# Kernel tuning notes

Hardware: AMD Instinct MI355X
Metric: run time of the kernel (lower is better)

## Reference

```python
import jax, jax.numpy as jnp
import numpy as np

GAMMA = 1.0

def setup_inputs() -> dict:
    key = jax.random.key(0)
    kx, ky = jax.random.split(key)
    x = jax.random.normal(kx, (8192, 512), dtype=jnp.float32)
    y = jax.random.normal(ky, (8192, 512), dtype=jnp.float32)
    return {"x": x, "y": y}

def reference(x, y):
    # RBF kernel K[i,j] = exp(-gamma * ||x_i - y_j||^2)
    # O(N*M*D) broadcasted diff tensor (128GB at these sizes).
    x_sq = jnp.sum(x * x, axis=-1)                      # [N]
    y_sq = jnp.sum(y * y, axis=-1)                      # [M]
    xy = jnp.einsum('nd,md->nm', x, y)                  # [N,M] GEMM
    sq_norm = x_sq[:, None] + y_sq[None, :] - 2.0 * xy
    sq_norm = jnp.maximum(sq_norm, 0.0)                 # guard fp cancellation
    return jnp.exp(-GAMMA * sq_norm)
```

## Files before the change

kernel.cpp:

```cpp
#include <hip/hip_runtime.h>


typedef int i32x8 __attribute__((ext_vector_type(8)));
typedef float f32x16 __attribute__((ext_vector_type(16)));

#define NROWS 8192
#define DIM 512
#define NKT 4

__device__ __forceinline__ unsigned char f2e4m3(float f) {
  unsigned u = __float_as_uint(f);
  unsigned sign = (u >> 24) & 0x80u;
  int e = (int)((u >> 23) & 0xFF);
  unsigned m = u & 0x7FFFFFu;
  if (e >= 127 + 9) return sign | 0x7E;
  if (e < 127 - 6) {
    if (e < 127 - 10) return (unsigned char)sign;
    unsigned full = 0x800000u | m;
    int div = 20 + (127 - 6 - e);
    unsigned q = full >> div;
    unsigned rem = full & ((1u << div) - 1u);
    unsigned half = 1u << (div - 1);
    q += (rem > half) || (rem == half && (q & 1));
    return (unsigned char)(sign | q);
  }
  unsigned q = m >> 20;
  unsigned rem = m & 0xFFFFFu;
  q += (rem > 0x80000u) || (rem == 0x80000u && (q & 1));
  unsigned ef = (unsigned)(e - 120);
  if (q == 8) { q = 0; ef++; }
  if (ef > 15 || (ef == 15 && q == 7)) return sign | 0x7E;
  return (unsigned char)(sign | (ef << 3) | q);
}

__device__ __forceinline__ void gload_lds16(const void* g, void* l) {
  __builtin_amdgcn_global_load_lds(
      (const __attribute__((address_space(1))) void*)g,
      (__attribute__((address_space(3))) void*)l, 16, 0, 0);
}

__device__ __forceinline__ f32x16 mfma_mx(i32x8 a, i32x8 b, f32x16 c) {
  return __builtin_amdgcn_mfma_scale_f32_32x32x64_f8f6f4(
      a, b, c, 0, 0, 0, 0x7F7F7F7Fu, 0, 0x7F7F7F7Fu);
}

__device__ __forceinline__ i32x8 lds_frag8(const unsigned char* hb, int R, int s0) {
  const int r7 = R & 7;
  int4 lo = *(const int4*)(hb + R * 128 + ((s0 ^ r7) << 4));
  int4 hi = *(const int4*)(hb + R * 128 + (((s0 + 1) ^ r7) << 4));
  i32x8 v;
  v[0] = lo.x; v[1] = lo.y; v[2] = lo.z; v[3] = lo.w;
  v[4] = hi.x; v[5] = hi.y; v[6] = hi.z; v[7] = hi.w;
  return v;
}

__global__ void rbf_prep(const float* __restrict__ x, const float* __restrict__ y,
                         unsigned char* __restrict__ xb, unsigned char* __restrict__ yb,
                         float* __restrict__ xsq, float* __restrict__ ysq) {
  int wave = threadIdx.x >> 6;
  int lane = threadIdx.x & 63;
  int row = blockIdx.x * 4 + wave;
  const float* src;
  unsigned char* dst;
  float* sq;
  int r;
  if (row < NROWS) { src = x; dst = xb; sq = xsq; r = row; }
  else             { src = y; dst = yb; sq = ysq; r = row - NROWS; }

  const float4* p = (const float4*)(src + (size_t)r * DIM);
  float4 v0 = p[lane * 2];
  float4 v1 = p[lane * 2 + 1];
  float s = v0.x * v0.x + v0.y * v0.y + v0.z * v0.z + v0.w * v0.w
          + v1.x * v1.x + v1.y * v1.y + v1.z * v1.z + v1.w * v1.w;

  union { uint2 u; unsigned char b[8]; } o;
  o.b[0] = f2e4m3(v0.x); o.b[1] = f2e4m3(v0.y);
  o.b[2] = f2e4m3(v0.z); o.b[3] = f2e4m3(v0.w);
  o.b[4] = f2e4m3(v1.x); o.b[5] = f2e4m3(v1.y);
  o.b[6] = f2e4m3(v1.z); o.b[7] = f2e4m3(v1.w);
  *(uint2*)(dst + (size_t)r * DIM + lane * 8) = o.u;

  #pragma unroll
  for (int off = 32; off > 0; off >>= 1) s += __shfl_down(s, off);
  if (lane == 0) sq[r] = s;
}

__global__ __launch_bounds__(512, 2) void rbf_gemm(
    const unsigned char* __restrict__ xb, const unsigned char* __restrict__ yb,
    const float* __restrict__ xsq, const float* __restrict__ ysq,
    float* __restrict__ out) {
  __shared__ __align__(16) unsigned char lds[2][2][2][128 * 128];

  const int t = threadIdx.x;
  const int lane = t & 63;
  const int w = t >> 6;
  const int wr = w >> 2;
  const int wc = w & 3;
  const int l31 = lane & 31;
  const int hi2 = lane >> 5;

  const int bx = blockIdx.x & 31;
  const int by = blockIdx.x >> 5;
  const size_t arow0 = (size_t)by * 256;
  const size_t brow0 = (size_t)bx * 256;

#define STAGE_HALF(d, ab, h, kt)                                            \
  {                                                                         \
    const unsigned char* gsrc_ = (ab) ? yb : xb;                            \
    const size_t grow0_ = ((ab) ? brow0 : arow0) + (h) * 128;               \
    _Pragma("unroll")                                                       \
    for (int r_ = 0; r_ < 2; ++r_) {                                        \
      const int c_ = r_ * 512 + t;                       \
      const int row_ = c_ >> 3;                                 \
      const int ss_ = c_ & 7;                                               \
      gload_lds16(gsrc_ + (grow0_ + row_) * DIM + (kt) * 128 +              \
                      ((ss_ ^ (row_ & 7)) << 4),                            \
                  &lds[d][ab][h][c_ * 16]);                                 \
    }                                                                       \
  }

#define MFMA_Q(afr, bfr, nt)                                                \
  _Pragma("unroll")                                                         \
  for (int m_ = 0; m_ < 4; ++m_)                                            \
    acc[m_][nt] = mfma_mx(afr[m_], bfr[nt], acc[m_][nt]);

  f32x16 acc[4][2] = {};

  STAGE_HALF(0, 0, 0, 0);
  STAGE_HALF(0, 0, 1, 0);
  STAGE_HALF(0, 1, 0, 0);
  STAGE_HALF(0, 1, 1, 0);
  STAGE_HALF(1, 0, 0, 1);
  STAGE_HALF(1, 0, 1, 1);
  asm volatile("s_waitcnt vmcnt(4)" ::: "memory");
  __builtin_amdgcn_sched_barrier(0);
  __builtin_amdgcn_s_barrier();

  #pragma unroll
  for (int kt = 0; kt < NKT; ++kt) {
    const int d = kt & 1;
    const unsigned char* Ah = lds[d][0][wr];
    const unsigned char* Bh = lds[d][1][wc >> 1];
    const int Rb = (wc & 1) * 64;

    const bool stB = kt + 1 < NKT;
    const bool stA = kt + 2 < NKT;
    const int dB = (kt + 1) & 1;

    i32x8 a0[4], a1[4], b0[2], b1[2];

    #pragma unroll
    for (int m = 0; m < 4; ++m) a0[m] = lds_frag8(Ah, m * 32 + l31, hi2 * 2);
    #pragma unroll
    for (int n = 0; n < 2; ++n)
      b0[n] = lds_frag8(Bh, Rb + n * 32 + l31, hi2 * 2);
    if (stB) STAGE_HALF(dB, 1, 0, kt + 1);
    __builtin_amdgcn_s_barrier();
    asm volatile("s_waitcnt lgkmcnt(0)" ::: "memory");
    __builtin_amdgcn_sched_barrier(0);
    __builtin_amdgcn_s_setprio(1);
    MFMA_Q(a0, b0, 0);
    __builtin_amdgcn_s_setprio(0);
    __builtin_amdgcn_s_barrier();

    #pragma unroll
    for (int m = 0; m < 4; ++m)
      a1[m] = lds_frag8(Ah, m * 32 + l31, 4 + hi2 * 2);
    #pragma unroll
    for (int n = 0; n < 2; ++n)
      b1[n] = lds_frag8(Bh, Rb + n * 32 + l31, 4 + hi2 * 2);
    if (stB) STAGE_HALF(dB, 1, 1, kt + 1);
    __builtin_amdgcn_s_barrier();
    asm volatile("s_waitcnt lgkmcnt(0)" ::: "memory");
    __builtin_amdgcn_sched_barrier(0);
    __builtin_amdgcn_s_setprio(1);
    MFMA_Q(a0, b0, 1);
    __builtin_amdgcn_s_setprio(0);
    __builtin_amdgcn_s_barrier();

    if (stA) STAGE_HALF(d, 0, 0, kt + 2);
    __builtin_amdgcn_s_barrier();
    __builtin_amdgcn_s_setprio(1);
    MFMA_Q(a1, b1, 0);
    __builtin_amdgcn_s_setprio(0);
    __builtin_amdgcn_s_barrier();

    if (stA) STAGE_HALF(d, 0, 1, kt + 2);
    __builtin_amdgcn_s_barrier();
    __builtin_amdgcn_s_setprio(1);
    MFMA_Q(a1, b1, 1);
    __builtin_amdgcn_s_setprio(0);
    if (stA) {
      asm volatile("s_waitcnt vmcnt(4)" ::: "memory");
    } else if (stB) {
      asm volatile("s_waitcnt vmcnt(0)" ::: "memory");
    }
    __builtin_amdgcn_sched_barrier(0);
    if (kt + 1 < NKT) __builtin_amdgcn_s_barrier();
  }

  const size_t orow0 = arow0 + wr * 128;
  const size_t ocol0 = brow0 + wc * 64;

  float ysv[2];
  #pragma unroll
  for (int n = 0; n < 2; ++n) ysv[n] = ysq[ocol0 + n * 32 + l31];

  #pragma unroll
  for (int mt = 0; mt < 4; ++mt) {
    #pragma unroll
    for (int j = 0; j < 16; ++j) {
      const int rl = (j & 3) + 8 * (j >> 2) + 4 * hi2;
      const size_t row = orow0 + mt * 32 + rl;
      const float xsv = xsq[row];
      #pragma unroll
      for (int n = 0; n < 2; ++n) {
        float v = xsv + ysv[n] - 2.0f * acc[mt][n][j];
        v = fmaxf(v, 0.0f);
        out[row * (size_t)NROWS + ocol0 + n * 32 + l31] = __expf(-v);
      }
    }
  }
}

__global__ void rbf_naive(const float* __restrict__ x, const float* __restrict__ y,
                          float* __restrict__ out) {
  int j = blockIdx.x * 16 + (threadIdx.x & 15);
  int i = blockIdx.y * 16 + (threadIdx.x >> 4);
  const float4* xp = (const float4*)(x + (size_t)i * DIM);
  const float4* yp = (const float4*)(y + (size_t)j * DIM);
  float s = 0.f;
  for (int k = 0; k < DIM / 4; ++k) {
    float4 a = xp[k], b = yp[k];
    float d0 = a.x - b.x, d1 = a.y - b.y, d2 = a.z - b.z, d3 = a.w - b.w;
    s += d0 * d0 + d1 * d1 + d2 * d2 + d3 * d3;
  }
  out[(size_t)i * NROWS + j] = __expf(-fmaxf(s, 0.0f));
}

extern "C" void kernel_launch(void* const* d_in, const int* in_sizes, int n_in,
                              void* d_out, int out_size, void* d_ws, size_t ws_size,
                              hipStream_t stream) {
  const float* x = (const float*)d_in[0];
  const float* y = (const float*)d_in[1];
  float* out = (float*)d_out;

  const size_t need = (size_t)8 * 1024 * 1024 + 64 * 1024;
  if (ws_size >= need) {
    unsigned char* xb = (unsigned char*)d_ws;
    unsigned char* yb = xb + (size_t)NROWS * DIM;
    float* xsq = (float*)((char*)d_ws + (size_t)8 * 1024 * 1024);
    float* ysq = xsq + NROWS;

    rbf_prep<<<(2 * NROWS) / 4, 256, 0, stream>>>(x, y, xb, yb, xsq, ysq);
    rbf_gemm<<<(NROWS / 256) * (NROWS / 256), 512, 0, stream>>>(xb, yb, xsq, ysq, out);
  } else {
    dim3 grid(NROWS / 16, NROWS / 16);
    rbf_naive<<<grid, 256, 0, stream>>>(x, y, out);
  }
}
```

Baseline: 88.49 us.

## Shrink GEMM tile to 128x128 with simple double-buffered pipeline and XCD-aware block remap

Changes the output tile from 256x256 with 512 threads to 128x128 with 256 threads, giving 4096 blocks instead of 1024. The hand-tuned ping-pong schedule with setprio and partial vmcnt waits is replaced by a plain double buffer with __syncthreads. Block IDs are remapped across the 8 XCDs so neighbouring tiles land on the same XCD for L2 reuse. The kernel is dominated by writing the 256MB fp32 output, so more, smaller blocks may balance the store traffic better. The cost is more redundant operand loads and less overlap between loads and MFMAs.

After: 93.30 us. +5.4%, slower.

```diff
diff --git a/kernel.cpp b/kernel.cpp
--- a/kernel.cpp
+++ b/kernel.cpp
@@ -44,10 +44,10 @@
       a, b, c, 0, 0, 0, 0x7F7F7F7Fu, 0, 0x7F7F7F7Fu);
 }
 
-__device__ __forceinline__ i32x8 lds_frag8(const unsigned char* hb, int R, int s0) {
+__device__ __forceinline__ i32x8 lds_frag8(const unsigned char* tb, int R, int s0) {
   const int r7 = R & 7;
-  int4 lo = *(const int4*)(hb + R * 128 + ((s0 ^ r7) << 4));
-  int4 hi = *(const int4*)(hb + R * 128 + (((s0 + 1) ^ r7) << 4));
+  int4 lo = *(const int4*)(tb + R * 128 + ((s0 ^ r7) << 4));
+  int4 hi = *(const int4*)(tb + R * 128 + (((s0 + 1) ^ r7) << 4));
   i32x8 v;
   v[0] = lo.x; v[1] = lo.y; v[2] = lo.z; v[3] = lo.w;
   v[4] = hi.x; v[5] = hi.y; v[6] = hi.z; v[7] = hi.w;
@@ -85,139 +85,99 @@
   if (lane == 0) sq[r] = s;
 }
 
-__global__ __launch_bounds__(512, 2) void rbf_gemm(
+__global__ __launch_bounds__(256, 2) void rbf_gemm(
     const unsigned char* __restrict__ xb, const unsigned char* __restrict__ yb,
     const float* __restrict__ xsq, const float* __restrict__ ysq,
     float* __restrict__ out) {
-  __shared__ __align__(16) unsigned char lds[2][2][2][128 * 128];
+  __shared__ __align__(16) unsigned char lds[2][2][128 * 128];
 
   const int t = threadIdx.x;
   const int lane = t & 63;
   const int w = t >> 6;
-  const int wr = w >> 2;
-  const int wc = w & 3;
+  const int wr = w >> 1;
+  const int wc = w & 1;
   const int l31 = lane & 31;
   const int hi2 = lane >> 5;
 
-  const int bx = blockIdx.x & 31;
-  const int by = blockIdx.x >> 5;
-  const size_t arow0 = (size_t)by * 256;
-  const size_t brow0 = (size_t)bx * 256;
-
-#define STAGE_HALF(d, ab, h, kt)                                            \
+  const int bid = ((int)blockIdx.x & 7) * 512 + ((int)blockIdx.x >> 3);
+  const int bx = bid & 63;
+  const int by = bid >> 6;
+  const size_t arow0 = (size_t)by * 128;
+  const size_t brow0 = (size_t)bx * 128;
+
+#define STAGE_T(d, ab, kt)                                                  \
   {                                                                         \
     const unsigned char* gsrc_ = (ab) ? yb : xb;                            \
-    const size_t grow0_ = ((ab) ? brow0 : arow0) + (h) * 128;               \
+    const size_t grow0_ = (ab) ? brow0 : arow0;                             \
     _Pragma("unroll")                                                       \
-    for (int r_ = 0; r_ < 2; ++r_) {                                        \
-      const int c_ = r_ * 512 + t;                       \
+    for (int q_ = 0; q_ < 4; ++q_) {                                        \
+      const int c_ = q_ * 256 + t;                       \
       const int row_ = c_ >> 3;                                 \
       const int ss_ = c_ & 7;                                               \
       gload_lds16(gsrc_ + (grow0_ + row_) * DIM + (kt) * 128 +              \
                       ((ss_ ^ (row_ & 7)) << 4),                            \
-                  &lds[d][ab][h][c_ * 16]);                                 \
+                  &lds[d][ab][c_ * 16]);                                    \
     }                                                                       \
   }
 
-#define MFMA_Q(afr, bfr, nt)                                                \
-  _Pragma("unroll")                                                         \
-  for (int m_ = 0; m_ < 4; ++m_)                                            \
-    acc[m_][nt] = mfma_mx(afr[m_], bfr[nt], acc[m_][nt]);
-
-  f32x16 acc[4][2] = {};
-
-  STAGE_HALF(0, 0, 0, 0);
-  STAGE_HALF(0, 0, 1, 0);
-  STAGE_HALF(0, 1, 0, 0);
-  STAGE_HALF(0, 1, 1, 0);
-  STAGE_HALF(1, 0, 0, 1);
-  STAGE_HALF(1, 0, 1, 1);
-  asm volatile("s_waitcnt vmcnt(4)" ::: "memory");
-  __builtin_amdgcn_sched_barrier(0);
-  __builtin_amdgcn_s_barrier();
+  f32x16 acc[2][2] = {};
+
+  STAGE_T(0, 0, 0);
+  STAGE_T(0, 1, 0);
+  __syncthreads();
 
   #pragma unroll
   for (int kt = 0; kt < NKT; ++kt) {
     const int d = kt & 1;
-    const unsigned char* Ah = lds[d][0][wr];
-    const unsigned char* Bh = lds[d][1][wc >> 1];
-    const int Rb = (wc & 1) * 64;
-
-    const bool stB = kt + 1 < NKT;
-    const bool stA = kt + 2 < NKT;
-    const int dB = (kt + 1) & 1;
-
-    i32x8 a0[4], a1[4], b0[2], b1[2];
-
-    #pragma unroll
-    for (int m = 0; m < 4; ++m) a0[m] = lds_frag8(Ah, m * 32 + l31, hi2 * 2);
-    #pragma unroll
-    for (int n = 0; n < 2; ++n)
-      b0[n] = lds_frag8(Bh, Rb + n * 32 + l31, hi2 * 2);
-    if (stB) STAGE_HALF(dB, 1, 0, kt + 1);
-    __builtin_amdgcn_s_barrier();
-    asm volatile("s_waitcnt lgkmcnt(0)" ::: "memory");
-    __builtin_amdgcn_sched_barrier(0);
-    __builtin_amdgcn_s_setprio(1);
-    MFMA_Q(a0, b0, 0);
-    __builtin_amdgcn_s_setprio(0);
-    __builtin_amdgcn_s_barrier();
-
-    #pragma unroll
-    for (int m = 0; m < 4; ++m)
-      a1[m] = lds_frag8(Ah, m * 32 + l31, 4 + hi2 * 2);
-    #pragma unroll
-    for (int n = 0; n < 2; ++n)
-      b1[n] = lds_frag8(Bh, Rb + n * 32 + l31, 4 + hi2 * 2);
-    if (stB) STAGE_HALF(dB, 1, 1, kt + 1);
-    __builtin_amdgcn_s_barrier();
-    asm volatile("s_waitcnt lgkmcnt(0)" ::: "memory");
-    __builtin_amdgcn_sched_barrier(0);
-    __builtin_amdgcn_s_setprio(1);
-    MFMA_Q(a0, b0, 1);
-    __builtin_amdgcn_s_setprio(0);
-    __builtin_amdgcn_s_barrier();
-
-    if (stA) STAGE_HALF(d, 0, 0, kt + 2);
-    __builtin_amdgcn_s_barrier();
-    __builtin_amdgcn_s_setprio(1);
-    MFMA_Q(a1, b1, 0);
-    __builtin_amdgcn_s_setprio(0);
-    __builtin_amdgcn_s_barrier();
-
-    if (stA) STAGE_HALF(d, 0, 1, kt + 2);
-    __builtin_amdgcn_s_barrier();
-    __builtin_amdgcn_s_setprio(1);
-    MFMA_Q(a1, b1, 1);
-    __builtin_amdgcn_s_setprio(0);
-    if (stA) {
-      asm volatile("s_waitcnt vmcnt(4)" ::: "memory");
-    } else if (stB) {
-      asm volatile("s_waitcnt vmcnt(0)" ::: "memory");
+    if (kt + 1 < NKT) {
+      STAGE_T(d ^ 1, 0, kt + 1);
+      STAGE_T(d ^ 1, 1, kt + 1);
     }
-    __builtin_amdgcn_sched_barrier(0);
-    if (kt + 1 < NKT) __builtin_amdgcn_s_barrier();
-  }
-
-  const size_t orow0 = arow0 + wr * 128;
+
+    const unsigned char* At = lds[d][0];
+    const unsigned char* Bt = lds[d][1];
+    i32x8 a[2][2], b[2][2];
+    #pragma unroll
+    for (int mt = 0; mt < 2; ++mt)
+      #pragma unroll
+      for (int ks = 0; ks < 2; ++ks)
+        a[mt][ks] = lds_frag8(At, wr * 64 + mt * 32 + l31, ks * 4 + hi2 * 2);
+    #pragma unroll
+    for (int nt = 0; nt < 2; ++nt)
+      #pragma unroll
+      for (int ks = 0; ks < 2; ++ks)
+        b[nt][ks] = lds_frag8(Bt, wc * 64 + nt * 32 + l31, ks * 4 + hi2 * 2);
+
+    #pragma unroll
+    for (int ks = 0; ks < 2; ++ks)
+      #pragma unroll
+      for (int mt = 0; mt < 2; ++mt)
+        #pragma unroll
+        for (int nt = 0; nt < 2; ++nt)
+          acc[mt][nt] = mfma_mx(a[mt][ks], b[nt][ks], acc[mt][nt]);
+
+    if (kt + 1 < NKT) __syncthreads();
+  }
+
+  const size_t orow0 = arow0 + wr * 64;
   const size_t ocol0 = brow0 + wc * 64;
 
   float ysv[2];
   #pragma unroll
-  for (int n = 0; n < 2; ++n) ysv[n] = ysq[ocol0 + n * 32 + l31];
-
-  #pragma unroll
-  for (int mt = 0; mt < 4; ++mt) {
+  for (int nt = 0; nt < 2; ++nt) ysv[nt] = ysq[ocol0 + nt * 32 + l31];
+
+  #pragma unroll
+  for (int mt = 0; mt < 2; ++mt) {
     #pragma unroll
     for (int j = 0; j < 16; ++j) {
       const int rl = (j & 3) + 8 * (j >> 2) + 4 * hi2;
       const size_t row = orow0 + mt * 32 + rl;
       const float xsv = xsq[row];
       #pragma unroll
-      for (int n = 0; n < 2; ++n) {
-        float v = xsv + ysv[n] - 2.0f * acc[mt][n][j];
+      for (int nt = 0; nt < 2; ++nt) {
+        float v = xsv + ysv[nt] - 2.0f * acc[mt][nt][j];
         v = fmaxf(v, 0.0f);
-        out[row * (size_t)NROWS + ocol0 + n * 32 + l31] = __expf(-v);
+        out[row * (size_t)NROWS + ocol0 + nt * 32 + l31] = __expf(-v);
       }
     }
   }
@@ -253,7 +213,7 @@
     float* ysq = xsq + NROWS;
 
     rbf_prep<<<(2 * NROWS) / 4, 256, 0, stream>>>(x, y, xb, yb, xsq, ysq);
-    rbf_gemm<<<(NROWS / 256) * (NROWS / 256), 512, 0, stream>>>(xb, yb, xsq, ysq, out);
+    rbf_gemm<<<(NROWS / 128) * (NROWS / 128), 256, 0, stream>>>(xb, yb, xsq, ysq, out);
   } else {
     dim3 grid(NROWS / 16, NROWS / 16);
     rbf_naive<<<grid, 256, 0, stream>>>(x, y, out);
```
